# Optimization experiments

Measured on AMD Instinct MI355X. Metric: run time of the kernel, lower is better.

## Reference

```python
import jax, jax.numpy as jnp
import numpy as np

GROUP = 16
IN_F = 4096
OUT_F = 4096
FP4_LEVELS = jnp.array([0.0, 0.5, 1.0, 1.5, 2.0, 3.0, 4.0, 6.0], dtype=jnp.float32)
# midpoints between consecutive fp4 magnitudes (round-to-nearest boundaries)
FP4_MIDS = jnp.array([0.25, 0.75, 1.25, 1.75, 2.5, 3.5, 5.0], dtype=jnp.float32)

def _e4m3_pos_table():
    bits = np.arange(127)  # positive e4m3 values, excluding NaN pattern 127
    e = bits >> 3
    m = bits & 7
    vals = np.where(e == 0, (m / 8.0) * 2.0 ** -6, (1.0 + m / 8.0) * 2.0 ** (e - 7.0))
    return jnp.asarray(vals, dtype=jnp.float32)

E4M3_POS = _e4m3_pos_table()

def e4m3_decode(bits):
    # bits: int array holding e4m3 bit patterns
    s = (bits >> 7) & 1
    e = ((bits >> 3) & 15).astype(jnp.float32)
    m = (bits & 7).astype(jnp.float32)
    mag = jnp.where(e == 0, (m / 8.0) * (2.0 ** -6), (1.0 + m / 8.0) * jnp.exp2(e - 7.0))
    return jnp.where(s == 1, -mag, mag).astype(jnp.float32)

def e4m3_round(x):
    # round non-negative x to nearest representable e4m3 value (returns float)
    x = jnp.clip(x, 0.0, 448.0)
    idx = jnp.clip(jnp.searchsorted(E4M3_POS, x), 1, 126)
    lo = E4M3_POS[idx - 1]
    hi = E4M3_POS[idx]
    return jnp.where(x - lo <= hi - x, lo, hi)

def fp4_decode(code):
    mag = FP4_LEVELS[code & 7]
    return jnp.where(code >= 8, -mag, mag)

def fp4_round(y):
    # round to nearest E2M1 value; clamp magnitude to 6
    a = jnp.minimum(jnp.abs(y), 6.0)
    idx = jnp.searchsorted(FP4_MIDS, a, side='right')
    return jnp.sign(y) * FP4_LEVELS[idx]

def nvfp4_quant_dequant(x2d, input_scale):
    # activation quantization: per-16 block e4m3 scale on top of per-tensor scale
    M, K = x2d.shape
    xb = x2d.reshape(M, K // GROUP, GROUP)
    amax = jnp.max(jnp.abs(xb), axis=-1, keepdims=True)
    bscale = e4m3_round(amax / (6.0 * input_scale))  # decoded e4m3 block scale
    eff = bscale * input_scale
    safe = jnp.where(eff > 0, eff, 1.0)
    q = fp4_round(xb / safe)
    return (q * eff).reshape(M, K)

def dequant_weight(weight, weight_scale, weight_scale_2):
    lo = weight & 15
    hi = (weight >> 4) & 15
    codes = jnp.stack([lo, hi], axis=-1).reshape(OUT_F, IN_F)  # [out, in]
    w = fp4_decode(codes)
    bs = e4m3_decode(weight_scale)  # [out, in//16]
    scale = jnp.repeat(bs, GROUP, axis=-1) * weight_scale_2  # [out, in]
    return w * scale

def setup_inputs() -> dict:
    key = jax.random.key(0)
    k1, k2, k3 = jax.random.split(key, 3)
    x = jax.random.normal(k1, (4, 2048, IN_F), dtype=jnp.float32)
    weight = jax.random.randint(k2, (OUT_F, IN_F // 2), 0, 256, dtype=jnp.int32)
    # e4m3 bit patterns with exponent in [4, 9], sign 0 -> scales ~[0.125, 3.75]
    weight_scale = jax.random.randint(k3, (OUT_F, IN_F // GROUP), 32, 80, dtype=jnp.int32)
    weight_scale_2 = jnp.array([0.02], dtype=jnp.float32)
    input_scale = jnp.array([0.01], dtype=jnp.float32)
    return {"x": x, "weight": weight, "weight_scale": weight_scale,
            "weight_scale_2": weight_scale_2, "input_scale": input_scale}

def reference(x, weight, weight_scale, weight_scale_2, input_scale):
    in_shape = x.shape
    x2d = x.reshape(-1, in_shape[-1])
    xd = nvfp4_quant_dequant(x2d, input_scale)           # quantize+dequant activations
    w = dequant_weight(weight, weight_scale, weight_scale_2)  # dequant fp4 weights
    out = jnp.einsum('mk,nk->mn', xd, w)                 # F.linear
    return out.reshape(*in_shape[:-1], OUT_F)
```

## Files before the change

kernel.cpp:

```cpp
#include <hip/hip_runtime.h>
#include <stdint.h>

#define IN_F  4096
#define OUT_F 4096
#define MROWS 8192

typedef __bf16 bf16x8 __attribute__((ext_vector_type(8)));
typedef float  f32x4  __attribute__((ext_vector_type(4)));


__device__ __forceinline__ float e4m3_round_dev(float x) {
    x = fminf(x, 448.0f);
    float lo, hi;
    if (x < 0.015625f) {
        const float step = 0.001953125f;
        lo = floorf(x * 512.0f) * step;
        hi = lo + step;
    } else {
        unsigned u = __float_as_uint(x);
        int E = (int)((u >> 23) & 0xFF) - 127;
        float step = __uint_as_float((unsigned)(E + 124) << 23);
        lo = floorf(x / step) * step;
        hi = lo + step;
    }
    return (x - lo <= hi - x) ? lo : hi;
}

__device__ __forceinline__ float e4m3_decode_dev(int bits) {
    int e = (bits >> 3) & 15;
    int m = bits & 7;
    float mag;
    if (e == 0) mag = (float)m * 0.001953125f;
    else        mag = (1.0f + (float)m * 0.125f) * __uint_as_float((unsigned)(e + 120) << 23);
    return (bits & 0x80) ? -mag : mag;
}

__device__ __forceinline__ float fp4_round_dev(float y) {
    float a = fminf(fabsf(y), 6.0f);
    float v;
    if (a < 1.75f) {
        if (a < 0.75f) v = (a < 0.25f) ? 0.0f : 0.5f;
        else           v = (a < 1.25f) ? 1.0f : 1.5f;
    } else {
        if (a < 3.5f)  v = (a < 2.5f) ? 2.0f : 3.0f;
        else           v = (a < 5.0f) ? 4.0f : 6.0f;
    }
    return copysignf(v, y);
}

__device__ __forceinline__ float fp4_decode_dev(int c) {
    int e = (c >> 1) & 3, m = c & 1;
    float mag = (e == 0) ? 0.5f * (float)m
                         : (1.0f + 0.5f * (float)m) * __uint_as_float((unsigned)(e + 126) << 23);
    return (c & 8) ? -mag : mag;
}

__device__ __forceinline__ unsigned pack_bf16x2(float a, float b) {
    return (__float_as_uint(a) >> 16) | ((__float_as_uint(b) >> 16) << 16);
}

__global__ __launch_bounds__(256) void quant_act_kernel(
    const float* __restrict__ x, const float* __restrict__ in_scale,
    unsigned short* __restrict__ Aq)
{
    int g = blockIdx.x * 256 + threadIdx.x;
    const float isc = in_scale[0];
    const float4* xp = (const float4*)x + (size_t)g * 4;
    float4 v0 = xp[0], v1 = xp[1], v2 = xp[2], v3 = xp[3];
    float f[16] = { v0.x, v0.y, v0.z, v0.w, v1.x, v1.y, v1.z, v1.w,
                    v2.x, v2.y, v2.z, v2.w, v3.x, v3.y, v3.z, v3.w };
    float amax = 0.0f;
    #pragma unroll
    for (int i = 0; i < 16; i++) amax = fmaxf(amax, fabsf(f[i]));

    float bscale = e4m3_round_dev(amax / (6.0f * isc));
    float eff = bscale * isc;
    float safe = (eff > 0.0f) ? eff : 1.0f;

    unsigned out[8];
    #pragma unroll
    for (int i = 0; i < 8; i++) {
        float a0 = fp4_round_dev(f[2 * i]     / safe) * bscale;
        float a1 = fp4_round_dev(f[2 * i + 1] / safe) * bscale;
        out[i] = pack_bf16x2(a0, a1);
    }
    uint4* dst = (uint4*)(Aq + (size_t)g * 16);
    dst[0] = make_uint4(out[0], out[1], out[2], out[3]);
    dst[1] = make_uint4(out[4], out[5], out[6], out[7]);
}

__global__ __launch_bounds__(256) void dequant_w_kernel(
    const int* __restrict__ wq, const int* __restrict__ wsb,
    unsigned short* __restrict__ Wd)
{
    int g = blockIdx.x * 256 + threadIdx.x;
    float scale = e4m3_decode_dev(wsb[g]);
    const int4* wp = (const int4*)wq + (size_t)g * 2;
    int4 b0 = wp[0], b1 = wp[1];
    int bytes[8] = { b0.x, b0.y, b0.z, b0.w, b1.x, b1.y, b1.z, b1.w };
    unsigned out[8];
    #pragma unroll
    for (int i = 0; i < 8; i++) {
        int by = bytes[i];
        float v0 = fp4_decode_dev(by & 15) * scale;
        float v1 = fp4_decode_dev((by >> 4) & 15) * scale;
        out[i] = pack_bf16x2(v0, v1);
    }
    uint4* dst = (uint4*)(Wd + (size_t)g * 16);
    dst[0] = make_uint4(out[0], out[1], out[2], out[3]);
    dst[1] = make_uint4(out[4], out[5], out[6], out[7]);
}

__device__ __forceinline__ void gload16(const void* g, void* l) {
    __builtin_amdgcn_global_load_lds((__attribute__((address_space(1))) void*)g,
                                     (__attribute__((address_space(3))) void*)l,
                                     16, 0, 0);
}

__global__ __launch_bounds__(256) void gemm_kernel(
    const unsigned short* __restrict__ A, const unsigned short* __restrict__ B,
    float* __restrict__ C, const float* __restrict__ isc,
    const float* __restrict__ ws2)
{
    __shared__ unsigned short As[128 * 32];
    __shared__ unsigned short Bs[128 * 32];

    const int tid  = threadIdx.x;
    const int lane = tid & 63;
    const int w    = tid >> 6;
    const int wm   = w >> 1, wn = w & 1;
    const int bm   = blockIdx.y, bn = blockIdx.x;

    const int c0 = tid, c1 = tid + 256;
    const char* pA0 = (const char*)(A + (size_t)(bm * 128 + (c0 >> 2)) * IN_F + (c0 & 3) * 8);
    const char* pA1 = (const char*)(A + (size_t)(bm * 128 + (c1 >> 2)) * IN_F + (c1 & 3) * 8);
    const char* pB0 = (const char*)(B + (size_t)(bn * 128 + (c0 >> 2)) * IN_F + (c0 & 3) * 8);
    const char* pB1 = (const char*)(B + (size_t)(bn * 128 + (c1 >> 2)) * IN_F + (c1 & 3) * 8);
    char* lA0 = (char*)As + (w * 64) * 16;
    char* lA1 = (char*)As + (256 + w * 64) * 16;
    char* lB0 = (char*)Bs + (w * 64) * 16;
    char* lB1 = (char*)Bs + (256 + w * 64) * 16;

    f32x4 acc[4][4];
    #pragma unroll
    for (int i = 0; i < 4; i++)
        #pragma unroll
        for (int j = 0; j < 4; j++)
            acc[i][j] = (f32x4){0.f, 0.f, 0.f, 0.f};

    const int l16 = lane & 15, quad = lane >> 4;
    const char* aBase = (const char*)As + (wm * 64 + l16) * 64 + quad * 16;
    const char* bBase = (const char*)Bs + (wn * 64 + l16) * 64 + quad * 16;

    for (int k = 0; k < IN_F; k += 32) {
        gload16(pA0, lA0); gload16(pA1, lA1);
        gload16(pB0, lB0); gload16(pB1, lB1);
        pA0 += 64; pA1 += 64; pB0 += 64; pB1 += 64;
        __syncthreads();

        bf16x8 af[4], bf[4];
        #pragma unroll
        for (int i = 0; i < 4; i++) {
            af[i] = *(const bf16x8*)(aBase + i * 16 * 64);
            bf[i] = *(const bf16x8*)(bBase + i * 16 * 64);
        }
        #pragma unroll
        for (int i = 0; i < 4; i++)
            #pragma unroll
            for (int j = 0; j < 4; j++)
                acc[i][j] = __builtin_amdgcn_mfma_f32_16x16x32_bf16(af[i], bf[j], acc[i][j], 0, 0, 0);
        __syncthreads();
    }

    const float s = isc[0] * ws2[0];
    #pragma unroll
    for (int i = 0; i < 4; i++) {
        int row0 = bm * 128 + wm * 64 + i * 16 + quad * 4;
        #pragma unroll
        for (int j = 0; j < 4; j++) {
            int col = bn * 128 + wn * 64 + j * 16 + l16;
            float* cp = C + (size_t)row0 * OUT_F + col;
            #pragma unroll
            for (int r = 0; r < 4; r++)
                cp[(size_t)r * OUT_F] = acc[i][j][r] * s;
        }
    }
}

extern "C" void kernel_launch(void* const* d_in, const int* in_sizes, int n_in,
                              void* d_out, int out_size, void* d_ws, size_t ws_size,
                              hipStream_t stream) {
    const float* x   = (const float*)d_in[0];
    const int*   wq  = (const int*)d_in[1];
    const int*   wsb = (const int*)d_in[2];
    const float* ws2 = (const float*)d_in[3];
    const float* isc = (const float*)d_in[4];
    float* out = (float*)d_out;

    unsigned short* Aq = (unsigned short*)d_ws;
    unsigned short* Wd = (unsigned short*)d_ws + (size_t)MROWS * IN_F;

    quant_act_kernel<<<8192, 256, 0, stream>>>(x, isc, Aq);
    dequant_w_kernel<<<4096, 256, 0, stream>>>(wq, wsb, Wd);
    gemm_kernel<<<dim3(32, 64), 256, 0, stream>>>(Aq, Wd, out, isc, ws2);

    (void)in_sizes; (void)n_in; (void)out_size; (void)ws_size;
}
```

Measured before the change: 541.5 us.

## Double GEMM K-tile to 64 with XOR-swizzled LDS layout; replace divides with reciprocals

The GEMM main loop now stages a 64-wide K slice per iteration instead of 32. This halves the number of barrier pairs and gives each sync interval twice the MFMA work. The LDS layout XOR-swizzles 16-byte chunks by row so fragment reads avoid bank conflicts. The activation quantizer and e4m3 rounding swap per-element divisions for multiplications by a precomputed reciprocal or power-of-two inverse, which could change rounding slightly for the non-power-of-two divisor. LDS use doubles to 32KB per block, which may reduce occupancy.

```diff
diff --git a/kernel.cpp b/kernel.cpp
--- a/kernel.cpp
+++ b/kernel.cpp
@@ -13,14 +13,14 @@
     x = fminf(x, 448.0f);
     float lo, hi;
     if (x < 0.015625f) {
-        const float step = 0.001953125f;
-        lo = floorf(x * 512.0f) * step;
-        hi = lo + step;
+        lo = floorf(x * 512.0f) * 0.001953125f;
+        hi = lo + 0.001953125f;
     } else {
         unsigned u = __float_as_uint(x);
         int E = (int)((u >> 23) & 0xFF) - 127;
-        float step = __uint_as_float((unsigned)(E + 124) << 23);
-        lo = floorf(x / step) * step;
+        float step  = __uint_as_float((unsigned)(E + 124) << 23);
+        float istep = __uint_as_float((unsigned)(130 - E) << 23);
+        lo = floorf(x * istep) * step;
         hi = lo + step;
     }
     return (x - lo <= hi - x) ? lo : hi;
@@ -76,12 +76,13 @@
     float bscale = e4m3_round_dev(amax / (6.0f * isc));
     float eff = bscale * isc;
     float safe = (eff > 0.0f) ? eff : 1.0f;
+    float inv = 1.0f / safe;
 
     unsigned out[8];
     #pragma unroll
     for (int i = 0; i < 8; i++) {
-        float a0 = fp4_round_dev(f[2 * i]     / safe) * bscale;
-        float a1 = fp4_round_dev(f[2 * i + 1] / safe) * bscale;
+        float a0 = fp4_round_dev(f[2 * i]     * inv) * bscale;
+        float a1 = fp4_round_dev(f[2 * i + 1] * inv) * bscale;
         out[i] = pack_bf16x2(a0, a1);
     }
     uint4* dst = (uint4*)(Aq + (size_t)g * 16);
@@ -122,8 +123,8 @@
     float* __restrict__ C, const float* __restrict__ isc,
     const float* __restrict__ ws2)
 {
-    __shared__ unsigned short As[128 * 32];
-    __shared__ unsigned short Bs[128 * 32];
+    __shared__ unsigned short As[128 * 64];
+    __shared__ unsigned short Bs[128 * 64];
 
     const int tid  = threadIdx.x;
     const int lane = tid & 63;
@@ -131,15 +132,18 @@
     const int wm   = w >> 1, wn = w & 1;
     const int bm   = blockIdx.y, bn = blockIdx.x;
 
-    const int c0 = tid, c1 = tid + 256;
-    const char* pA0 = (const char*)(A + (size_t)(bm * 128 + (c0 >> 2)) * IN_F + (c0 & 3) * 8);
-    const char* pA1 = (const char*)(A + (size_t)(bm * 128 + (c1 >> 2)) * IN_F + (c1 & 3) * 8);
-    const char* pB0 = (const char*)(B + (size_t)(bn * 128 + (c0 >> 2)) * IN_F + (c0 & 3) * 8);
-    const char* pB1 = (const char*)(B + (size_t)(bn * 128 + (c1 >> 2)) * IN_F + (c1 & 3) * 8);
-    char* lA0 = (char*)As + (w * 64) * 16;
-    char* lA1 = (char*)As + (256 + w * 64) * 16;
-    char* lB0 = (char*)Bs + (w * 64) * 16;
-    char* lB1 = (char*)Bs + (256 + w * 64) * 16;
+    const char* pA[4]; const char* pB[4];
+    char* lA[4]; char* lB[4];
+    #pragma unroll
+    for (int i = 0; i < 4; i++) {
+        int c   = tid + 256 * i;
+        int row = c >> 3;
+        int kc  = (c & 7) ^ (row & 7);
+        pA[i] = (const char*)(A + (size_t)(bm * 128 + row) * IN_F + kc * 8);
+        pB[i] = (const char*)(B + (size_t)(bn * 128 + row) * IN_F + kc * 8);
+        lA[i] = (char*)As + c * 16;
+        lB[i] = (char*)Bs + c * 16;
+    }
 
     f32x4 acc[4][4];
     #pragma unroll
@@ -149,26 +153,33 @@
             acc[i][j] = (f32x4){0.f, 0.f, 0.f, 0.f};
 
     const int l16 = lane & 15, quad = lane >> 4;
-    const char* aBase = (const char*)As + (wm * 64 + l16) * 64 + quad * 16;
-    const char* bBase = (const char*)Bs + (wn * 64 + l16) * 64 + quad * 16;
-
-    for (int k = 0; k < IN_F; k += 32) {
-        gload16(pA0, lA0); gload16(pA1, lA1);
-        gload16(pB0, lB0); gload16(pB1, lB1);
-        pA0 += 64; pA1 += 64; pB0 += 64; pB1 += 64;
+    const int x7  = l16 & 7;
+    const char* aRow = (const char*)As + (wm * 64 + l16) * 128;
+    const char* bRow = (const char*)Bs + (wn * 64 + l16) * 128;
+
+    for (int k = 0; k < IN_F; k += 64) {
+        #pragma unroll
+        for (int i = 0; i < 4; i++) {
+            gload16(pA[i], lA[i]); gload16(pB[i], lB[i]);
+            pA[i] += 128; pB[i] += 128;
+        }
         __syncthreads();
 
-        bf16x8 af[4], bf[4];
-        #pragma unroll
-        for (int i = 0; i < 4; i++) {
-            af[i] = *(const bf16x8*)(aBase + i * 16 * 64);
-            bf[i] = *(const bf16x8*)(bBase + i * 16 * 64);
+        #pragma unroll
+        for (int h = 0; h < 2; h++) {
+            const int sw = (((h << 2) | quad) ^ x7) * 16;
+            bf16x8 af[4], bf[4];
+            #pragma unroll
+            for (int i = 0; i < 4; i++) {
+                af[i] = *(const bf16x8*)(aRow + i * 16 * 128 + sw);
+                bf[i] = *(const bf16x8*)(bRow + i * 16 * 128 + sw);
+            }
+            #pragma unroll
+            for (int i = 0; i < 4; i++)
+                #pragma unroll
+                for (int j = 0; j < 4; j++)
+                    acc[i][j] = __builtin_amdgcn_mfma_f32_16x16x32_bf16(af[i], bf[j], acc[i][j], 0, 0, 0);
         }
-        #pragma unroll
-        for (int i = 0; i < 4; i++)
-            #pragma unroll
-            for (int j = 0; j < 4; j++)
-                acc[i][j] = __builtin_amdgcn_mfma_f32_16x16x32_bf16(af[i], bf[j], acc[i][j], 0, 0, 0);
         __syncthreads();
     }
 
```

New measurement: 510.9 us. 5.6% less time.
